# Performance work log

Hardware: AMD Instinct MI355X
Metric: run time of the kernel (lower is better)

The kernel has to match this reference:

```python
import jax, jax.numpy as jnp
import numpy as np

N_E = 1024
E_DIM = 256
N_TOK = 65536
BETA = 0.25


def setup_inputs() -> dict:
    key = jax.random.key(0)
    k1, k2 = jax.random.split(key)
    z = jax.random.normal(k1, (N_TOK, E_DIM), dtype=jnp.float32)
    # nn.Embedding weight, init uniform(-1/n_e, 1/n_e) in the original; use normal-like scale via uniform
    W = jax.random.uniform(k2, (N_E, E_DIM), dtype=jnp.float32, minval=-1.0 / N_E, maxval=1.0 / N_E)
    return {"z": z, "W": W}


def reference(z, W):
    # cosine distance: d = -normalize(z) @ normalize(W).T  -> (N, n_e)
    zn = z / jnp.linalg.norm(z, axis=-1, keepdims=True)
    Wn = W / jnp.linalg.norm(W, axis=-1, keepdims=True)
    d = -jnp.einsum('nd,ed->ne', zn, Wn)
    min_idx = jnp.argmin(d, axis=1)                       # (N,)
    z_q = W[min_idx]                                       # (N, e_dim)
    # commitment / codebook loss with straight-through style detaches
    loss = jnp.mean((jax.lax.stop_gradient(z) - z_q) ** 2) \
         + BETA * jnp.mean((z - jax.lax.stop_gradient(z_q)) ** 2)
    # pos_indices = unique(min_idx) (sorted); neg = np.delete(arange(n_e), pos) (sorted)
    # emb = cat(W[pos], W[neg]); reproduce with a stable argsort on membership mask
    pos_mask = jnp.zeros((N_E,), dtype=bool).at[min_idx].set(True)
    order = jnp.argsort(jnp.logical_not(pos_mask), stable=True)  # pos (sorted) first, then neg (sorted)
    emb = W[order]                                         # (n_e, e_dim)
    label = pos_mask[order].astype(z.dtype)                # (n_e,)
    return emb, label, loss
```

## Files before the change

### kernel.cpp

```cpp
#include <hip/hip_runtime.h>
#include <hip/hip_bf16.h>
#include <math.h>


typedef unsigned short u16;
typedef unsigned int   u32;
typedef unsigned long long u64;
typedef __attribute__((ext_vector_type(8))) short short8;
typedef __attribute__((ext_vector_type(4))) float f32x4;

#define N_E   1024
#define E_DIM 256
#define N_TOK 65536
#define BETA  0.25f
#define CAPL  24
#define CAPG  8
#define D_ADM 0.08f
#define D_FIL 0.09f

#define WS_INVNORM 0
#define WS_NORMW   4096
#define WS_MASK    8192
#define WS_LACC    12288
#define WS_WCNT    14336
#define WS_WCNT2   14340
#define WS_WSW     16384
#define WS_CNT     540672
#define WS_CAND    802816
#define WS_WLIST   1851392
#define WS_WLIST2  2113536

static __device__ __forceinline__ u16 f2bf(float f) {
    u32 u = __float_as_uint(f);
    return (u16)((u + 0x7FFFu + ((u >> 16) & 1u)) >> 16);
}
static __device__ __forceinline__ u32 pk2bf(float a, float b) {
    __hip_bfloat162 p = __float22bfloat162_rn(make_float2(a, b));
    return *reinterpret_cast<u32*>(&p);
}
static __device__ __forceinline__ u32 keyenc(float f) {
    u32 u = __float_as_uint(f);
    return u ^ (u32)(((int)u >> 31) | 0x80000000);
}
static __device__ __forceinline__ float keydec(u32 k) {
    u32 u = (k & 0x80000000u) ? (k ^ 0x80000000u) : ~k;
    return __uint_as_float(u);
}

__global__ void k_prep(const float* __restrict__ W, u16* __restrict__ Wsw,
                       float* __restrict__ inv_norm, float* __restrict__ normW,
                       int* __restrict__ mask, double* __restrict__ lacc,
                       u32* __restrict__ wcnt, u32* __restrict__ wcnt2) {
    const int n = blockIdx.x;
    const int l = threadIdx.x;
    const float4 v = reinterpret_cast<const float4*>(W + (size_t)n * E_DIM)[l];
    float s = v.x * v.x + v.y * v.y + v.z * v.z + v.w * v.w;
#pragma unroll
    for (int sh = 1; sh < 64; sh <<= 1) s += __shfl_xor(s, sh, 64);
    const float nw = sqrtf(s), inv = 1.0f / nw;
    if (l == 0) {
        inv_norm[n] = inv; normW[n] = nw; mask[n] = 0;
        if (n < 256) lacc[n] = 0.0;
        if (n == 0) { *wcnt = 0u; *wcnt2 = 0u; }
    }
    const int o = l >> 1;
    const int kc = o >> 2, q = o & 3;
    const size_t base =
        (((((size_t)(n >> 7) * 8 + kc) * 8 + ((n >> 4) & 7)) * 64 +
          (q * 16 + (n & 15))) * 8) + (l & 1) * 4;
    u16* dst = Wsw + base;
    dst[0] = f2bf(v.x * inv);
    dst[1] = f2bf(v.y * inv);
    dst[2] = f2bf(v.z * inv);
    dst[3] = f2bf(v.w * inv);
}

__global__ __launch_bounds__(512, 4)
void k_score(const float* __restrict__ z, const u16* __restrict__ Wsw,
             const float* __restrict__ normW, u16* __restrict__ cand_g,
             u32* __restrict__ cnt_g, int* __restrict__ mask,
             u32* __restrict__ wlist, u32* __restrict__ wcnt,
             u32* __restrict__ wlist2, u32* __restrict__ wcnt2,
             double* __restrict__ lacc) {
    __shared__ __align__(16) u16 A_sw[32768];
    __shared__ u32 bestk[128];
    __shared__ u32 cnt[128];
    __shared__ u32 slots[128 * CAPL];

    const int t    = threadIdx.x;
    const int lane = t & 63;
    const int w    = t >> 6;
    const size_t tok_base = (size_t)blockIdx.x * 128;

    if (t < 128) { bestk[t] = 0u; cnt[t] = 0u; }

    float ssq = 0.f;
#pragma unroll
    for (int i = 0; i < 8; i++) {
        const int m = ((i & 1) << 6) | (w << 3) | (lane & 7);
        const int o = ((i >> 1) << 3) | (lane >> 3);
        const float* zp = z + (tok_base + m) * E_DIM + o * 8;
        const float4 v0 = reinterpret_cast<const float4*>(zp)[0];
        const float4 v1 = reinterpret_cast<const float4*>(zp)[1];
        ssq += v0.x * v0.x + v0.y * v0.y + v0.z * v0.z + v0.w * v0.w
             + v1.x * v1.x + v1.y * v1.y + v1.z * v1.z + v1.w * v1.w;
        uint4 d;
        d.x = pk2bf(v0.x, v0.y);
        d.y = pk2bf(v0.z, v0.w);
        d.z = pk2bf(v1.x, v1.y);
        d.w = pk2bf(v1.z, v1.w);
        const int kc = o >> 2, q = o & 3, col = m & 15, mt = m >> 4;
        *reinterpret_cast<uint4*>(A_sw + ((size_t)((kc * 8 + mt) * 64 + q * 16 + col)) * 8) = d;
    }
#pragma unroll
    for (int sh = 1; sh < 64; sh <<= 1) ssq += __shfl_xor(ssq, sh, 64);
    if (lane == 0) atomicAdd(&lacc[(blockIdx.x * 8 + w) & 255], (double)ssq);
    __syncthreads();

    const int mq = w >> 2;
    const int nq = w & 3;
    const int q = lane >> 4, col = lane & 15;
    const u16* wb = Wsw + ((size_t)((nq >> 1) * 64 + (nq & 1) * 4)) * 512
                        + (size_t)lane * 8;

    f32x4 acc[4][4];

#define ZERO_ACC() { _Pragma("unroll") for (int mi = 0; mi < 4; mi++) \
    _Pragma("unroll") for (int ni = 0; ni < 4; ni++) { \
        f32x4 zf = {0.f, 0.f, 0.f, 0.f}; acc[mi][ni] = zf; } }

#define KLOOP(NB2) { \
    __builtin_amdgcn_s_setprio(1); \
    _Pragma("unroll 4") \
    for (int kc = 0; kc < 8; kc++) { \
        short8 bf[4], af[4]; \
        _Pragma("unroll") for (int ni = 0; ni < 4; ni++) \
            bf[ni] = *reinterpret_cast<const short8*>( \
                wb + (size_t)((NB2) * 128 + kc * 8 + ni) * 512); \
        _Pragma("unroll") for (int mi = 0; mi < 4; mi++) \
            af[mi] = *reinterpret_cast<const short8*>( \
                A_sw + ((size_t)((kc * 8 + mq * 4 + mi) * 64 + lane)) * 8); \
        _Pragma("unroll") for (int mi = 0; mi < 4; mi++) \
        _Pragma("unroll") for (int ni = 0; ni < 4; ni++) \
            acc[mi][ni] = __builtin_amdgcn_mfma_f32_16x16x32_bf16( \
                af[mi], bf[ni], acc[mi][ni], 0, 0, 0); } \
    __builtin_amdgcn_s_setprio(0); }

#define ADMIT(NB2, DO_MAX) { \
    _Pragma("unroll") for (int mi = 0; mi < 4; mi++) \
    _Pragma("unroll") for (int r = 0; r < 4; r++) { \
        const int tk = mq * 64 + mi * 16 + q * 4 + r; \
        const float thr = keydec(bestk[tk]) - D_ADM; \
        _Pragma("unroll") for (int ni = 0; ni < 4; ni++) { \
            const float v = acc[mi][ni][r]; \
            if (v >= thr) { \
                if (DO_MAX) atomicMax(&bestk[tk], keyenc(v)); \
                const int code = ((NB2) * 16 + nq * 4 + ni) * 16 + col; \
                const u32 sl = atomicAdd(&cnt[tk], 1u); \
                if (sl < CAPL) { \
                    const float vc = fminf(fmaxf((v + 16.f) * 2048.f, 0.f), 65535.f); \
                    slots[tk * CAPL + sl] = ((u32)vc << 16) | (u32)code; \
                } } } } }

    ZERO_ACC();
    KLOOP(0);
#pragma unroll
    for (int mi = 0; mi < 4; mi++)
#pragma unroll
        for (int r = 0; r < 4; r++) {
            float m0 = fmaxf(fmaxf(acc[mi][0][r], acc[mi][1][r]),
                             fmaxf(acc[mi][2][r], acc[mi][3][r]));
#pragma unroll
            for (int sh = 1; sh < 16; sh <<= 1)
                m0 = fmaxf(m0, __shfl_xor(m0, sh, 64));
            if (col == 0)
                atomicMax(&bestk[mq * 64 + mi * 16 + q * 4 + r], keyenc(m0));
        }
    __syncthreads();
    ADMIT(0, 0);

#pragma unroll 1
    for (int nb2 = 1; nb2 < 4; nb2++) {
        ZERO_ACC();
        KLOOP(nb2);
        ADMIT(nb2, 1);
    }
#undef ZERO_ACC
#undef KLOOP
#undef ADMIT

    __syncthreads();
    if (t < 128) {
        const size_t tokg = tok_base + t;
        const u32 c = cnt[t];
        const float best = keydec(bestk[t]);
        bool amb = false, ovf = false;
        float xacc = 0.f;
        if (c > CAPL) {
            ovf = true;
        } else {
            const float thrf = best - D_FIL;
            u16 loc[CAPG]; u32 m = 0;
            for (u32 i = 0; i < c; i++) {
                const u32 s2 = slots[t * CAPL + i];
                const float ap = (float)(s2 >> 16) * (1.0f / 2048.0f) - 16.0f;
                if (ap >= thrf) { if (m < CAPG) loc[m] = (u16)(s2 & 0xFFFFu); m++; }
            }
            if (m == 1) {
                const int bi = loc[0];
                mask[bi] = 1;
                const float nw = normW[bi];
                xacc = fmaf(-2.0f * best, nw, nw * nw);
            } else if (m <= CAPG) {
                for (u32 i = 0; i < m; i++) cand_g[tokg * CAPG + i] = loc[i];
                cnt_g[tokg] = m; amb = true;
            } else {
                ovf = true;
            }
        }
        {
            const u64 bal = __ballot(amb);
            u32 base = 0;
            if (lane == 0 && bal) base = atomicAdd(wcnt, (u32)__popcll(bal));
            base = (u32)__shfl((int)base, 0, 64);
            if (amb) wlist[base + (u32)__popcll(bal & ((1ull << lane) - 1ull))] = (u32)tokg;
        }
        {
            const u64 bal = __ballot(ovf);
            u32 base = 0;
            if (lane == 0 && bal) base = atomicAdd(wcnt2, (u32)__popcll(bal));
            base = (u32)__shfl((int)base, 0, 64);
            if (ovf) wlist2[base + (u32)__popcll(bal & ((1ull << lane) - 1ull))] = (u32)tokg;
        }
        float xs = xacc;
#pragma unroll
        for (int sh = 1; sh < 64; sh <<= 1) xs += __shfl_xor(xs, sh, 64);
        if (lane == 0) atomicAdd(&lacc[(blockIdx.x * 2 + w) & 255], (double)xs);
    }
}

__global__ __launch_bounds__(256)
void k_pick(const float* __restrict__ z, const float* __restrict__ W,
            const float* __restrict__ inv_norm, const float* __restrict__ normW,
            const u16* __restrict__ cand_g, const u32* __restrict__ cnt_g,
            const u32* __restrict__ wlist, const u32* __restrict__ wcnt,
            const u32* __restrict__ wlist2, const u32* __restrict__ wcnt2,
            int* __restrict__ mask, double* __restrict__ lacc) {
    __shared__ float zrow[E_DIM];
    __shared__ float gbv[16], gbp[16];
    __shared__ int   gbi[16];
    const int t = threadIdx.x, lane = t & 63;
    const int gl = t & 15, grp = t >> 4;

    {
        const u32 total = *wcnt;
        float xs = 0.f;
        for (u32 i = blockIdx.x * 16 + grp; i < total; i += 1024 * 16) {
            const size_t tok = wlist[i];
            float4 zv[4];
#pragma unroll
            for (int j = 0; j < 4; j++)
                zv[j] = reinterpret_cast<const float4*>(z + tok * E_DIM)[j * 16 + gl];
            const int n_it = (int)cnt_g[tok];
            float bv = -3.4e38f, bp = 0.f;
            int bi = 0x7FFFFFFF;
#pragma unroll 1
            for (int k2 = 0; k2 < n_it; k2++) {
                const int c = (int)cand_g[tok * CAPG + k2];
                float p = 0.f;
#pragma unroll
                for (int j = 0; j < 4; j++) {
                    const float4 wv = reinterpret_cast<const float4*>(W + (size_t)c * E_DIM)[j * 16 + gl];
                    p += zv[j].x * wv.x + zv[j].y * wv.y + zv[j].z * wv.z + zv[j].w * wv.w;
                }
#pragma unroll
                for (int sh = 1; sh < 16; sh <<= 1) p += __shfl_xor(p, sh, 64);
                const float s = p * inv_norm[c];
                if (s > bv || (s == bv && c < bi)) { bv = s; bi = c; bp = p; }
            }
            if (gl == 0) {
                mask[bi] = 1;
                xs += fmaf(-2.0f, bp, normW[bi] * normW[bi]);
            }
        }
        xs += __shfl_xor(xs, 16, 64);
        xs += __shfl_xor(xs, 32, 64);
        if (lane == 0) atomicAdd(&lacc[(blockIdx.x * 4 + (t >> 6)) & 255], (double)xs);
    }

    {
        const u32 total2 = *wcnt2;
        for (u32 i = blockIdx.x; i < total2; i += 1024) {
            const size_t tok = wlist2[i];
            __syncthreads();
            zrow[t] = z[tok * E_DIM + t];
            __syncthreads();
            float4 zv[4];
#pragma unroll
            for (int j = 0; j < 4; j++)
                zv[j] = reinterpret_cast<const float4*>(zrow)[j * 16 + gl];
            float bv = -3.4e38f, bp = 0.f;
            int bi = 0x7FFFFFFF;
#pragma unroll 1
            for (int k2 = 0; k2 < 64; k2 += 2) {
                const int c0 = grp * 64 + k2, c1 = c0 + 1;
                float p0 = 0.f, p1 = 0.f;
#pragma unroll
                for (int j = 0; j < 4; j++) {
                    const float4 w0 = reinterpret_cast<const float4*>(W + (size_t)c0 * E_DIM)[j * 16 + gl];
                    const float4 w1 = reinterpret_cast<const float4*>(W + (size_t)c1 * E_DIM)[j * 16 + gl];
                    p0 += zv[j].x * w0.x + zv[j].y * w0.y + zv[j].z * w0.z + zv[j].w * w0.w;
                    p1 += zv[j].x * w1.x + zv[j].y * w1.y + zv[j].z * w1.z + zv[j].w * w1.w;
                }
#pragma unroll
                for (int sh = 1; sh < 16; sh <<= 1) {
                    p0 += __shfl_xor(p0, sh, 64);
                    p1 += __shfl_xor(p1, sh, 64);
                }
                const float s0 = p0 * inv_norm[c0];
                const float s1 = p1 * inv_norm[c1];
                if (s0 > bv || (s0 == bv && c0 < bi)) { bv = s0; bi = c0; bp = p0; }
                if (s1 > bv || (s1 == bv && c1 < bi)) { bv = s1; bi = c1; bp = p1; }
            }
            if (gl == 0) { gbv[grp] = bv; gbi[grp] = bi; gbp[grp] = bp; }
            __syncthreads();
            if (t == 0) {
                float fb = gbv[0], fp = gbp[0];
                int fi = gbi[0];
                for (int g2 = 1; g2 < 16; g2++) {
                    const float v2 = gbv[g2];
                    const int i2 = gbi[g2];
                    if (v2 > fb || (v2 == fb && i2 < fi)) { fb = v2; fi = i2; fp = gbp[g2]; }
                }
                mask[fi] = 1;
                atomicAdd(&lacc[tok & 255],
                          (double)fmaf(-2.0f, fp, normW[fi] * normW[fi]));
            }
        }
    }
}

__global__ __launch_bounds__(256)
void k_emit(const float* __restrict__ W, const int* __restrict__ mask,
            const double* __restrict__ lacc, float* __restrict__ out) {
    __shared__ int    redp[256], redt[256];
    __shared__ double dred[256];
    const int e = blockIdx.x;
    const int t = threadIdx.x;
    const int4 mv = reinterpret_cast<const int4*>(mask)[t];
    const int b = t * 4;
    redt[t] = mv.x + mv.y + mv.z + mv.w;
    redp[t] = (b + 0 < e ? mv.x : 0) + (b + 1 < e ? mv.y : 0) +
              (b + 2 < e ? mv.z : 0) + (b + 3 < e ? mv.w : 0);
    if (e == 0) dred[t] = lacc[t];
    __syncthreads();
#pragma unroll
    for (int s2 = 128; s2 > 0; s2 >>= 1) {
        if (t < s2) {
            redp[t] += redp[t + s2];
            redt[t] += redt[t + s2];
            if (e == 0) dred[t] += dred[t + s2];
        }
        __syncthreads();
    }
    const int prefix = redp[0], total = redt[0];
    const int m = mask[e];
    const int r = m ? prefix : (total + e - prefix);
    out[(size_t)r * E_DIM + t] = W[(size_t)e * E_DIM + t];
    if (t == 0) out[(size_t)N_E * E_DIM + r] = m ? 1.0f : 0.0f;
    if (e == 0 && t == 0) {
        const double mse = dred[0] / (double)((size_t)N_TOK * E_DIM);
        out[(size_t)N_E * E_DIM + N_E] = (float)((1.0 + (double)BETA) * mse);
    }
}

extern "C" void kernel_launch(void* const* d_in, const int* in_sizes, int n_in,
                              void* d_out, int out_size, void* d_ws, size_t ws_size,
                              hipStream_t stream) {
    const float* z = (const float*)d_in[0];
    const float* W = (const float*)d_in[1];
    float* out = (float*)d_out;
    char* ws = (char*)d_ws;

    float*  inv_norm = (float*)(ws + WS_INVNORM);
    float*  normW    = (float*)(ws + WS_NORMW);
    int*    mask     = (int*)(ws + WS_MASK);
    double* lacc     = (double*)(ws + WS_LACC);
    u32*    wcnt     = (u32*)(ws + WS_WCNT);
    u32*    wcnt2    = (u32*)(ws + WS_WCNT2);
    u16*    Wsw      = (u16*)(ws + WS_WSW);
    u32*    cnt      = (u32*)(ws + WS_CNT);
    u16*    cand     = (u16*)(ws + WS_CAND);
    u32*    wlist    = (u32*)(ws + WS_WLIST);
    u32*    wlist2   = (u32*)(ws + WS_WLIST2);

    k_prep <<<N_E, 64, 0, stream>>>(W, Wsw, inv_norm, normW, mask, lacc,
                                    wcnt, wcnt2);
    k_score<<<N_TOK / 128, 512, 0, stream>>>(z, Wsw, normW, cand, cnt, mask,
                                             wlist, wcnt, wlist2, wcnt2, lacc);
    k_pick <<<1024, 256, 0, stream>>>(z, W, inv_norm, normW, cand, cnt,
                                      wlist, wcnt, wlist2, wcnt2, mask, lacc);
    k_emit <<<N_E, 256, 0, stream>>>(W, mask, lacc, out);
}
```

Before: 153.8 us.

## Shrink score tile to 32 tokens per block and prefilter admission by row max

The scoring kernel now handles 32 tokens per block with 4 waves instead of 128 tokens with 8 waves. Each wave covers all 32 tokens for its quarter of the codebook, which cuts shared memory and accumulator registers and allows more resident blocks. The admission step first tests the max over four accumulators before doing per-element atomics, which reduces shared-memory atomic traffic. The trade-off is that each codebook B-fragment is reused across fewer tokens, so global and L2 traffic for the normalized codebook rises about fourfold.

```diff
diff --git a/kernel.cpp b/kernel.cpp
--- a/kernel.cpp
+++ b/kernel.cpp
@@ -17,6 +17,7 @@
 #define CAPG  8
 #define D_ADM 0.08f
 #define D_FIL 0.09f
+#define TPB   32
 
 #define WS_INVNORM 0
 #define WS_NORMW   4096
@@ -75,30 +76,30 @@
     dst[3] = f2bf(v.w * inv);
 }
 
-__global__ __launch_bounds__(512, 4)
+__global__ __launch_bounds__(256, 6)
 void k_score(const float* __restrict__ z, const u16* __restrict__ Wsw,
              const float* __restrict__ normW, u16* __restrict__ cand_g,
              u32* __restrict__ cnt_g, int* __restrict__ mask,
              u32* __restrict__ wlist, u32* __restrict__ wcnt,
              u32* __restrict__ wlist2, u32* __restrict__ wcnt2,
              double* __restrict__ lacc) {
-    __shared__ __align__(16) u16 A_sw[32768];
-    __shared__ u32 bestk[128];
-    __shared__ u32 cnt[128];
-    __shared__ u32 slots[128 * CAPL];
+    __shared__ __align__(16) u16 A_sw[8192];
+    __shared__ u32 bestk[TPB];
+    __shared__ u32 cnt[TPB];
+    __shared__ u32 slots[TPB * CAPL];
 
     const int t    = threadIdx.x;
     const int lane = t & 63;
     const int w    = t >> 6;
-    const size_t tok_base = (size_t)blockIdx.x * 128;
-
-    if (t < 128) { bestk[t] = 0u; cnt[t] = 0u; }
+    const size_t tok_base = (size_t)blockIdx.x * TPB;
+
+    if (t < TPB) { bestk[t] = 0u; cnt[t] = 0u; }
 
     float ssq = 0.f;
 #pragma unroll
-    for (int i = 0; i < 8; i++) {
-        const int m = ((i & 1) << 6) | (w << 3) | (lane & 7);
-        const int o = ((i >> 1) << 3) | (lane >> 3);
+    for (int i = 0; i < 4; i++) {
+        const int m = (w << 3) | (lane & 7);
+        const int o = (i << 3) | (lane >> 3);
         const float* zp = z + (tok_base + m) * E_DIM + o * 8;
         const float4 v0 = reinterpret_cast<const float4*>(zp)[0];
         const float4 v1 = reinterpret_cast<const float4*>(zp)[1];
@@ -110,22 +111,21 @@
         d.z = pk2bf(v1.x, v1.y);
         d.w = pk2bf(v1.z, v1.w);
         const int kc = o >> 2, q = o & 3, col = m & 15, mt = m >> 4;
-        *reinterpret_cast<uint4*>(A_sw + ((size_t)((kc * 8 + mt) * 64 + q * 16 + col)) * 8) = d;
+        *reinterpret_cast<uint4*>(A_sw + ((size_t)((kc * 2 + mt) * 64 + q * 16 + col)) * 8) = d;
     }
 #pragma unroll
     for (int sh = 1; sh < 64; sh <<= 1) ssq += __shfl_xor(ssq, sh, 64);
-    if (lane == 0) atomicAdd(&lacc[(blockIdx.x * 8 + w) & 255], (double)ssq);
+    if (lane == 0) atomicAdd(&lacc[(blockIdx.x * 4 + w) & 255], (double)ssq);
     __syncthreads();
 
-    const int mq = w >> 2;
-    const int nq = w & 3;
+    const int nq = w;
     const int q = lane >> 4, col = lane & 15;
     const u16* wb = Wsw + ((size_t)((nq >> 1) * 64 + (nq & 1) * 4)) * 512
                         + (size_t)lane * 8;
 
-    f32x4 acc[4][4];
-
-#define ZERO_ACC() { _Pragma("unroll") for (int mi = 0; mi < 4; mi++) \
+    f32x4 acc[2][4];
+
+#define ZERO_ACC() { _Pragma("unroll") for (int mi = 0; mi < 2; mi++) \
     _Pragma("unroll") for (int ni = 0; ni < 4; ni++) { \
         f32x4 zf = {0.f, 0.f, 0.f, 0.f}; acc[mi][ni] = zf; } }
 
@@ -133,39 +133,42 @@
     __builtin_amdgcn_s_setprio(1); \
     _Pragma("unroll 4") \
     for (int kc = 0; kc < 8; kc++) { \
-        short8 bf[4], af[4]; \
+        short8 bf[4], af[2]; \
         _Pragma("unroll") for (int ni = 0; ni < 4; ni++) \
             bf[ni] = *reinterpret_cast<const short8*>( \
                 wb + (size_t)((NB2) * 128 + kc * 8 + ni) * 512); \
-        _Pragma("unroll") for (int mi = 0; mi < 4; mi++) \
+        _Pragma("unroll") for (int mi = 0; mi < 2; mi++) \
             af[mi] = *reinterpret_cast<const short8*>( \
-                A_sw + ((size_t)((kc * 8 + mq * 4 + mi) * 64 + lane)) * 8); \
-        _Pragma("unroll") for (int mi = 0; mi < 4; mi++) \
+                A_sw + ((size_t)((kc * 2 + mi) * 64 + lane)) * 8); \
+        _Pragma("unroll") for (int mi = 0; mi < 2; mi++) \
         _Pragma("unroll") for (int ni = 0; ni < 4; ni++) \
             acc[mi][ni] = __builtin_amdgcn_mfma_f32_16x16x32_bf16( \
                 af[mi], bf[ni], acc[mi][ni], 0, 0, 0); } \
     __builtin_amdgcn_s_setprio(0); }
 
 #define ADMIT(NB2, DO_MAX) { \
-    _Pragma("unroll") for (int mi = 0; mi < 4; mi++) \
+    _Pragma("unroll") for (int mi = 0; mi < 2; mi++) \
     _Pragma("unroll") for (int r = 0; r < 4; r++) { \
-        const int tk = mq * 64 + mi * 16 + q * 4 + r; \
+        const int tk = mi * 16 + q * 4 + r; \
         const float thr = keydec(bestk[tk]) - D_ADM; \
-        _Pragma("unroll") for (int ni = 0; ni < 4; ni++) { \
-            const float v = acc[mi][ni][r]; \
-            if (v >= thr) { \
-                if (DO_MAX) atomicMax(&bestk[tk], keyenc(v)); \
-                const int code = ((NB2) * 16 + nq * 4 + ni) * 16 + col; \
-                const u32 sl = atomicAdd(&cnt[tk], 1u); \
-                if (sl < CAPL) { \
-                    const float vc = fminf(fmaxf((v + 16.f) * 2048.f, 0.f), 65535.f); \
-                    slots[tk * CAPL + sl] = ((u32)vc << 16) | (u32)code; \
-                } } } } }
+        const float vmax = fmaxf(fmaxf(acc[mi][0][r], acc[mi][1][r]), \
+                                 fmaxf(acc[mi][2][r], acc[mi][3][r])); \
+        if (vmax >= thr) { \
+            if (DO_MAX) atomicMax(&bestk[tk], keyenc(vmax)); \
+            _Pragma("unroll") for (int ni = 0; ni < 4; ni++) { \
+                const float v = acc[mi][ni][r]; \
+                if (v >= thr) { \
+                    const int code = ((NB2) * 16 + nq * 4 + ni) * 16 + col; \
+                    const u32 sl = atomicAdd(&cnt[tk], 1u); \
+                    if (sl < CAPL) { \
+                        const float vc = fminf(fmaxf((v + 16.f) * 2048.f, 0.f), 65535.f); \
+                        slots[tk * CAPL + sl] = ((u32)vc << 16) | (u32)code; \
+                    } } } } } }
 
     ZERO_ACC();
     KLOOP(0);
 #pragma unroll
-    for (int mi = 0; mi < 4; mi++)
+    for (int mi = 0; mi < 2; mi++)
 #pragma unroll
         for (int r = 0; r < 4; r++) {
             float m0 = fmaxf(fmaxf(acc[mi][0][r], acc[mi][1][r]),
@@ -174,7 +177,7 @@
             for (int sh = 1; sh < 16; sh <<= 1)
                 m0 = fmaxf(m0, __shfl_xor(m0, sh, 64));
             if (col == 0)
-                atomicMax(&bestk[mq * 64 + mi * 16 + q * 4 + r], keyenc(m0));
+                atomicMax(&bestk[mi * 16 + q * 4 + r], keyenc(m0));
         }
     __syncthreads();
     ADMIT(0, 0);
@@ -190,7 +193,7 @@
 #undef ADMIT
 
     __syncthreads();
-    if (t < 128) {
+    if (t < TPB) {
         const size_t tokg = tok_base + t;
         const u32 c = cnt[t];
         const float best = keydec(bestk[t]);
@@ -234,8 +237,8 @@
         }
         float xs = xacc;
 #pragma unroll
-        for (int sh = 1; sh < 64; sh <<= 1) xs += __shfl_xor(xs, sh, 64);
-        if (lane == 0) atomicAdd(&lacc[(blockIdx.x * 2 + w) & 255], (double)xs);
+        for (int sh = 1; sh < 32; sh <<= 1) xs += __shfl_xor(xs, sh, 64);
+        if (lane == 0) atomicAdd(&lacc[(blockIdx.x * 2) & 255], (double)xs);
     }
 }
 
@@ -396,7 +399,7 @@
 
     k_prep <<<N_E, 64, 0, stream>>>(W, Wsw, inv_norm, normW, mask, lacc,
                                     wcnt, wcnt2);
-    k_score<<<N_TOK / 128, 512, 0, stream>>>(z, Wsw, normW, cand, cnt, mask,
+    k_score<<<N_TOK / TPB, 256, 0, stream>>>(z, Wsw, normW, cand, cnt, mask,
                                              wlist, wcnt, wlist2, wcnt2, lacc);
     k_pick <<<1024, 256, 0, stream>>>(z, W, inv_norm, normW, cand, cnt,
                                       wlist, wcnt, wlist2, wcnt2, mask, lacc);
```

Measured after the change: 160.1 us. 4.1% more time.
